# Kernel optimization log

Hardware: AMD Instinct MI355X
Metric: run time of the kernel (lower is better)

Reference implementation:

```python
import jax, jax.numpy as jnp
import numpy as np

N = 100000
C = 64
E = 3200000


def setup_inputs() -> dict:
    key = jax.random.key(0)
    k1, k2, k3 = jax.random.split(key, 3)
    edge_index = jax.random.randint(k1, (2, E), 0, N, dtype=jnp.int64)
    # nn.Linear(num_nodes, out_channels): weight [C, N], bias [C]
    W = jax.random.normal(k2, (C, N), dtype=jnp.float32) * 0.01
    b = jax.random.normal(k3, (C,), dtype=jnp.float32) * 0.01
    return {"edge_index": edge_index, "W": W, "b": b}


def reference(edge_index, W, b):
    # logits = A @ W.T + b, with A the N x N COO adjacency built from edge_index.
    # Row r of A @ W.T = sum_{edges (r, c)} W[:, c], so this is a gather of
    # W.T rows at col, segment-summed over row (duplicate edges accumulate,
    # matching torch sparse COO semantics).
    n = W.shape[1]
    row = edge_index[0]
    col = edge_index[1]
    row = row - row.min()  # faithful to the original's row normalization
    Wt = W.T  # [N, C]
    gathered = Wt[col]  # [E, C]
    out = jax.ops.segment_sum(gathered, row, num_segments=n)  # [N, C]
    return out + b
```

## Files before the change

kernel.cpp:

```cpp
#include <hip/hip_runtime.h>


#define OVF_MAX (1 << 19)
#define NBKT 512
#define BSH 9
#define SLOTS 30
#define GT_STRIDE 16
#define SL 56
#define LROWS 196

typedef unsigned int uint2_ev __attribute__((ext_vector_type(2)));
typedef unsigned int uint4_ev __attribute__((ext_vector_type(4)));

__device__ __forceinline__ float bf16u_to_f(unsigned short u) {
    union { unsigned int i; float f; } x; x.i = ((unsigned int)u) << 16; return x.f;
}
__device__ __forceinline__ float bflo(unsigned int u) {
    union { unsigned int i; float f; } x; x.i = u << 16; return x.f;
}
__device__ __forceinline__ float bfhi(unsigned int u) {
    union { unsigned int i; float f; } x; x.i = u & 0xFFFF0000u; return x.f;
}

__global__ __launch_bounds__(1024) void LINK_detect_kernel(
    const unsigned int* __restrict__ words, int E, int* __restrict__ flags,
    int* __restrict__ gtail) {
    long long twoE = 2LL * E;
    int tid = threadIdx.x;
    unsigned int oddOr = 0u;
    int nscan = (int)(twoE < 8192 ? twoE : 8192);
    for (int i = tid; i < nscan; i += blockDim.x) {
        if (i & 1) oddOr |= words[i];
        long long j = twoE - 1 - i;
        if (j >= nscan && (j & 1)) oddOr |= words[j];
    }
    __shared__ unsigned int sred[16];
    for (int off = 32; off > 0; off >>= 1)
        oddOr |= (unsigned int)__shfl_down((int)oddOr, off, 64);
    int wid = tid >> 6;
    if ((tid & 63) == 0) sred[wid] = oddOr;
    __syncthreads();
    if (tid == 0) {
        unsigned int o = 0;
        for (int i = 0; i < (int)(blockDim.x >> 6); ++i) o |= sred[i];
        flags[0] = o ? 1 : 0;
        flags[1] = 0x7f7f7f7f;
        flags[8] = 0;
    }
    for (int k = tid; k < NBKT; k += blockDim.x) gtail[k * GT_STRIDE] = 0;
}

__global__ void LINK_transpose_kernel(const float* __restrict__ W,
                                      unsigned short* __restrict__ Wtb, int N) {
    __shared__ float tile[64][65];
    int n0 = blockIdx.x * 64;
    int lx = threadIdx.x & 63;
    int ly = threadIdx.x >> 6;
#pragma unroll
    for (int it = 0; it < 16; ++it) {
        int ch = ly + 4 * it;
        float v = 0.0f;
        if (n0 + lx < N) v = W[(size_t)ch * N + (n0 + lx)];
        tile[lx][ch] = v;
    }
    __syncthreads();
#pragma unroll
    for (int it = 0; it < 16; ++it) {
        int nn = ly + 4 * it;
        if (n0 + nn <= N) {
            union { float f; unsigned int i; } x; x.f = tile[nn][lx];
            unsigned int u = x.i;
            unsigned int r = (u + 0x7fffu + ((u >> 16) & 1u)) >> 16;
            Wtb[((size_t)(n0 + nn) << 6) + lx] = (unsigned short)r;
        }
    }
}

__global__ __launch_bounds__(1024, 8) void LINK_part_kernel(
    const unsigned int* __restrict__ words, int E, int N, int segcap,
    int* __restrict__ gtail, unsigned int* __restrict__ recs,
    int* __restrict__ ovf, int* __restrict__ flags) {
    __shared__ unsigned int lstage[NBKT * SLOTS];
    __shared__ int lcnt[NBKT];
    __shared__ int sred[16];
    int tid = threadIdx.x;
    int lane = tid & 63, wid = tid >> 6;
    for (int k = tid; k < NBKT; k += 1024) lcnt[k] = 0;
    __syncthreads();
    int isInt32 = flags[0];
    int mnr = 0x7f7f7f7f;
    long long P = ((long long)E + 1) >> 1;
    long long stride = (long long)gridDim.x * 1024;
    for (long long p = (long long)blockIdx.x * 1024 + tid; p < P; p += stride) {
        long long e0 = p << 1;
        int r0, c0, r1 = 0, c1 = 0;
        bool has1 = (e0 + 1 < E);
        if (isInt32) {
            if (has1) {
                uint2_ev rr = __builtin_nontemporal_load((const uint2_ev*)(words + e0));
                uint2_ev cc = __builtin_nontemporal_load((const uint2_ev*)(words + E + e0));
                r0 = (int)rr.x; r1 = (int)rr.y; c0 = (int)cc.x; c1 = (int)cc.y;
            } else {
                r0 = (int)words[e0]; c0 = (int)words[E + e0];
            }
        } else {
            if (has1) {
                uint4_ev rr = __builtin_nontemporal_load((const uint4_ev*)(words + (e0 << 1)));
                uint4_ev cc = __builtin_nontemporal_load((const uint4_ev*)(words + 2LL * E + (e0 << 1)));
                r0 = (int)rr.x; r1 = (int)rr.z; c0 = (int)cc.x; c1 = (int)cc.z;
            } else {
                r0 = (int)words[e0 << 1]; c0 = (int)words[2LL * E + (e0 << 1)];
            }
        }
#pragma unroll
        for (int u = 0; u < 2; ++u) {
            if (u && !has1) break;
            int r = u ? r1 : r0, c = u ? c1 : c0;
            mnr = min(mnr, r);
            if ((unsigned)r < (unsigned)N && (unsigned)c < (unsigned)N) {
                int k = r & (NBKT - 1);
                unsigned int rec = ((unsigned int)(r >> BSH) << 17) | (unsigned int)c;
                int pos = atomicAdd(&lcnt[k], 1);
                if (pos < SLOTS) {
                    lstage[k * SLOTS + pos] = rec;
                } else {
                    int g = atomicAdd(&gtail[k * GT_STRIDE], 1);
                    if (g < segcap) recs[(size_t)k * segcap + g] = rec;
                    else {
                        int oi = atomicAdd(&flags[8], 1);
                        if (oi < OVF_MAX) { ovf[2 * oi] = r; ovf[2 * oi + 1] = c; }
                    }
                }
            }
        }
    }
    __syncthreads();
    for (int k = wid; k < NBKT; k += 16) {
        int cnt = lcnt[k]; if (cnt > SLOTS) cnt = SLOTS;
        if (cnt > 0) {
            int g = 0;
            if (lane == 0) g = atomicAdd(&gtail[k * GT_STRIDE], cnt);
            g = __shfl(g, 0);
            if (lane < cnt) {
                int gg = g + lane;
                unsigned int rec = lstage[k * SLOTS + lane];
                if (gg < segcap) recs[(size_t)k * segcap + gg] = rec;
                else {
                    int oi = atomicAdd(&flags[8], 1);
                    if (oi < OVF_MAX) {
                        ovf[2 * oi] = (int)((rec >> 17) << BSH) | k;
                        ovf[2 * oi + 1] = (int)(rec & 0x1FFFF);
                    }
                }
            }
        }
    }
    for (int off = 32; off > 0; off >>= 1) mnr = min(mnr, __shfl_down(mnr, off, 64));
    if (lane == 0) sred[wid] = mnr;
    __syncthreads();
    if (tid == 0) {
        int m = sred[0];
        for (int i = 1; i < 16; ++i) m = min(m, sred[i]);
        atomicMin(&flags[1], m);
    }
}

__global__ __launch_bounds__(1024, 8) void LINK_bgather_kernel(
    const int* __restrict__ gtail, const unsigned int* __restrict__ recs, int segcap,
    const unsigned short* __restrict__ Wtb, const float* __restrict__ bias,
    float* __restrict__ out, int* __restrict__ flags, int* __restrict__ ovf, int N) {
    __shared__ __attribute__((aligned(16))) int lcols[LROWS * SL];
    __shared__ int lcnt[LROWS];
    int tid = threadIdx.x;
    int lane = tid & 63, wid = tid >> 6;
    int nloc = (N + NBKT - 1) >> BSH;
    for (int b = blockIdx.x; b < NBKT; b += gridDim.x) {
        __syncthreads();
        for (int k = tid; k < nloc; k += 1024) lcnt[k] = 0;
        __syncthreads();
        int len = gtail[b * GT_STRIDE]; if (len > segcap) len = segcap;
        const unsigned int* rp = recs + (size_t)b * segcap;
        for (int i = tid; i < len; i += 1024) {
            unsigned int rec = __builtin_nontemporal_load(rp + i);
            int lr = (int)(rec >> 17);
            int c = (int)(rec & 0x1FFFF);
            int pos = atomicAdd(&lcnt[lr], 1);
            if (pos < SL) {
                lcols[lr * SL + pos] = c;
            } else {
                int oi = atomicAdd(&flags[8], 1);
                if (oi < OVF_MAX) { ovf[2 * oi] = (lr << BSH) | b; ovf[2 * oi + 1] = c; }
            }
        }
        __syncthreads();
        if (tid < nloc) {
            int c0 = lcnt[tid]; if (c0 > SL) c0 = SL;
            if (c0 & 1) { lcols[tid * SL + c0] = N; ++c0; }
            lcnt[tid] = c0;
        }
        __syncthreads();
        int rmin = flags[1];
        int half = lane >> 5, ln = lane & 31;
        const unsigned int* __restrict__ W32 = (const unsigned int*)Wtb;
        float bv = bias[(ln << 1) + half];
        for (int lr = wid; lr < nloc; lr += 16) {
            int cnt = lcnt[lr];
            int base = lr * SL;
            float aL = 0.0f, aH = 0.0f;
            int j = 0;
            for (; j + 16 <= cnt; j += 16) {
                int4 q0 = *(const int4*)&lcols[base + j + (half << 2)];
                int4 q1 = *(const int4*)&lcols[base + j + 8 + (half << 2)];
                unsigned int u0 = W32[(((unsigned)q0.x) << 5) | ln];
                unsigned int u1 = W32[(((unsigned)q0.y) << 5) | ln];
                unsigned int u2 = W32[(((unsigned)q0.z) << 5) | ln];
                unsigned int u3 = W32[(((unsigned)q0.w) << 5) | ln];
                unsigned int u4 = W32[(((unsigned)q1.x) << 5) | ln];
                unsigned int u5 = W32[(((unsigned)q1.y) << 5) | ln];
                unsigned int u6 = W32[(((unsigned)q1.z) << 5) | ln];
                unsigned int u7 = W32[(((unsigned)q1.w) << 5) | ln];
                float l0 = (bflo(u0) + bflo(u1)) + (bflo(u2) + bflo(u3));
                float l1 = (bflo(u4) + bflo(u5)) + (bflo(u6) + bflo(u7));
                float h0 = (bfhi(u0) + bfhi(u1)) + (bfhi(u2) + bfhi(u3));
                float h1 = (bfhi(u4) + bfhi(u5)) + (bfhi(u6) + bfhi(u7));
                aL += l0 + l1;
                aH += h0 + h1;
            }
            for (; j + 8 <= cnt; j += 8) {
                int4 q = *(const int4*)&lcols[base + j + (half << 2)];
                unsigned int u0 = W32[(((unsigned)q.x) << 5) | ln];
                unsigned int u1 = W32[(((unsigned)q.y) << 5) | ln];
                unsigned int u2 = W32[(((unsigned)q.z) << 5) | ln];
                unsigned int u3 = W32[(((unsigned)q.w) << 5) | ln];
                aL += (bflo(u0) + bflo(u1)) + (bflo(u2) + bflo(u3));
                aH += (bfhi(u0) + bfhi(u1)) + (bfhi(u2) + bfhi(u3));
            }
            for (; j + 4 <= cnt; j += 4) {
                int2 q = *(const int2*)&lcols[base + j + (half << 1)];
                unsigned int u0 = W32[(((unsigned)q.x) << 5) | ln];
                unsigned int u1 = W32[(((unsigned)q.y) << 5) | ln];
                aL += bflo(u0) + bflo(u1);
                aH += bfhi(u0) + bfhi(u1);
            }
            for (; j + 2 <= cnt; j += 2) {
                int c = lcols[base + j + half];
                unsigned int u = W32[(((unsigned)c) << 5) | ln];
                aL += bflo(u);
                aH += bfhi(u);
            }
            aL += __shfl_xor(aL, 32, 64);
            aH += __shfl_xor(aH, 32, 64);
            int orow = (lr << BSH) + b - rmin;
            if ((unsigned)orow < (unsigned)N)
                out[((size_t)orow << 6) + (ln << 1) + half] = (half ? aH : aL) + bv;
        }
    }
}

__global__ void LINK_tail_kernel(float* __restrict__ out, const float* __restrict__ bias,
                                 const int* __restrict__ flags, const int* __restrict__ ovf,
                                 const unsigned short* __restrict__ Wtb, int N) {
    int rmin = flags[1];
    int nloc = (N + NBKT - 1) >> BSH;
    long long start = (long long)nloc * NBKT - (long long)rmin;
    if (start < 0) start = 0;
    if (start < N) {
        long long total = ((long long)N - start) * 64;
        long long base = start * 64;
        long long i0 = (long long)blockIdx.x * blockDim.x + threadIdx.x;
        long long stride = (long long)gridDim.x * blockDim.x;
        for (long long i = i0; i < total; i += stride) out[base + i] = bias[(int)(i & 63)];
    }
    int cnt = flags[8]; if (cnt > OVF_MAX) cnt = OVF_MAX;
    if (cnt == 0) return;
    int g = blockIdx.x * blockDim.x + threadIdx.x;
    int w = g >> 6, lane = g & 63;
    int nw = (gridDim.x * blockDim.x) >> 6;
    for (int i = w; i < cnt; i += nw) {
        int r = ovf[2 * i] - rmin;
        int c = ovf[2 * i + 1];
        if ((unsigned)r >= (unsigned)N || (unsigned)c >= (unsigned)N) continue;
        atomicAdd(&out[((size_t)r << 6) + lane], bf16u_to_f(Wtb[((size_t)c << 6) + lane]));
    }
}

__global__ void LINK_initout_kernel(float* __restrict__ out, const float* __restrict__ b,
                                    int total, int* __restrict__ flags) {
    int i = blockIdx.x * blockDim.x + threadIdx.x;
    if (i == 0) { flags[0] = 0; flags[1] = 0x7fffffff; flags[2] = 0x7fffffff; }
    if (i < total) out[i] = b[i & 63];
}

__global__ __launch_bounds__(256) void LINK_analyze_kernel(
    const unsigned int* __restrict__ words, int E, int* __restrict__ flags) {
    const uint4* __restrict__ w4 = (const uint4*)words;
    int tid = blockIdx.x * blockDim.x + threadIdx.x;
    int nth = gridDim.x * blockDim.x;
    int n1 = E >> 2;
    long long twoE = 2LL * E;
    int n2 = (int)(twoE >> 2);
    unsigned int oddOr = 0u;
    int mn32 = 0x7fffffff, mn64 = 0x7fffffff;
    for (int i = tid; i < n2; i += nth) {
        uint4 w = w4[i];
        oddOr |= (w.y | w.w);
        mn64 = min(mn64, min((int)w.x, (int)w.z));
        if (i < n1)
            mn32 = min(mn32, min(min((int)w.x, (int)w.y), min((int)w.z, (int)w.w)));
    }
    for (long long i = ((long long)n1 << 2) + tid; i < E; i += nth)
        mn32 = min(mn32, (int)words[i]);
    for (long long i = ((long long)n2 << 2) + tid; i < twoE; i += nth) {
        unsigned int w = words[i];
        if (i & 1) oddOr |= w; else mn64 = min(mn64, (int)w);
    }
    for (int off = 32; off > 0; off >>= 1) {
        oddOr |= (unsigned int)__shfl_down((int)oddOr, off, 64);
        mn32 = min(mn32, __shfl_down(mn32, off, 64));
        mn64 = min(mn64, __shfl_down(mn64, off, 64));
    }
    __shared__ int s_or[4], s_m32[4], s_m64[4];
    int wid = threadIdx.x >> 6;
    if ((threadIdx.x & 63) == 0) { s_or[wid] = (int)oddOr; s_m32[wid] = mn32; s_m64[wid] = mn64; }
    __syncthreads();
    if (threadIdx.x == 0) {
        int o = s_or[0] | s_or[1] | s_or[2] | s_or[3];
        int a = min(min(s_m32[0], s_m32[1]), min(s_m32[2], s_m32[3]));
        int d = min(min(s_m64[0], s_m64[1]), min(s_m64[2], s_m64[3]));
        if (o) atomicOr(&flags[0], 1);
        atomicMin(&flags[1], a);
        atomicMin(&flags[2], d);
    }
}

__global__ void LINK_scatter_kernel(const unsigned int* __restrict__ words, int E,
                                    const float* __restrict__ W,
                                    float* __restrict__ out,
                                    const int* __restrict__ flags, int N) {
    long long g = (long long)blockIdx.x * blockDim.x + threadIdx.x;
    int e = (int)(g >> 6);
    if (e >= E) return;
    int ch = (int)(g & 63);
    int r, c, rmin;
    if (flags[0]) { r = (int)words[e]; c = (int)words[E + e]; rmin = flags[1]; }
    else { r = (int)words[2LL * e]; c = (int)words[2LL * (E + e)]; rmin = flags[2]; }
    r -= rmin;
    if ((unsigned)r >= (unsigned)N || (unsigned)c >= (unsigned)N) return;
    atomicAdd(&out[((size_t)r << 6) + ch], W[(size_t)ch * N + c]);
}

static inline size_t align256(size_t x) { return (x + 255) & ~(size_t)255; }

extern "C" void kernel_launch(void* const* d_in, const int* in_sizes, int n_in,
                              void* d_out, int out_size, void* d_ws, size_t ws_size,
                              hipStream_t stream) {
    const unsigned int* words = (const unsigned int*)d_in[0];
    const float* W = (const float*)d_in[1];
    const float* b = (const float*)d_in[2];
    float* out = (float*)d_out;

    int E = in_sizes[0] / 2;
    int N = in_sizes[1] / 64;
    int total = out_size;

    size_t off_flags = 0;
    size_t off_wtb   = align256(off_flags + 256 * sizeof(int));
    size_t off_gtail = align256(off_wtb + (size_t)(N + 1) * 64 * sizeof(unsigned short));
    size_t off_ovf   = align256(off_gtail + (size_t)NBKT * GT_STRIDE * sizeof(int));
    size_t off_recs  = align256(off_ovf + (size_t)OVF_MAX * 2 * sizeof(int));

    int* flags = (int*)((char*)d_ws + off_flags);
    unsigned short* Wtb = (unsigned short*)((char*)d_ws + off_wtb);
    int* gtail = (int*)((char*)d_ws + off_gtail);
    int* ovf   = (int*)((char*)d_ws + off_ovf);
    unsigned int* recs = (unsigned int*)((char*)d_ws + off_recs);

    long long avail = (ws_size > off_recs)
        ? (long long)((ws_size - off_recs) / ((size_t)NBKT * sizeof(int))) : 0;
    int segcap = (int)(avail > 16384 ? 16384 : avail);
    int avg = E / NBKT + 1;
    int nloc = (N + NBKT - 1) >> BSH;
    bool useMain = (nloc <= LROWS) && (E > 0) &&
                   (segcap >= avg + avg / 8 + 64);

    if (useMain) {
        LINK_detect_kernel<<<1, 1024, 0, stream>>>(words, E, flags, gtail);
        LINK_transpose_kernel<<<(N + 64) / 64, 256, 0, stream>>>(W, Wtb, N);
        LINK_part_kernel<<<NBKT, 1024, 0, stream>>>(words, E, N, segcap,
                                                    gtail, recs, ovf, flags);
        LINK_bgather_kernel<<<NBKT, 1024, 0, stream>>>(gtail, recs, segcap, Wtb, b,
                                                       out, flags, ovf, N);
        LINK_tail_kernel<<<64, 256, 0, stream>>>(out, b, flags, ovf, Wtb, N);
    } else {
        LINK_initout_kernel<<<(total + 255) / 256, 256, 0, stream>>>(out, b, total, flags);
        LINK_analyze_kernel<<<256, 256, 0, stream>>>(words, E, flags);
        long long tthreads = (long long)E * 64;
        LINK_scatter_kernel<<<(int)((tthreads + 255) / 256), 256, 0, stream>>>(
            words, E, W, out, flags, N);
    }
}
```

Measured before the change: 196.7 us.

## Fuse detect into transpose kernel and fold tail work into gather's last block

Merges the single-block detect/init kernel into the transpose launch as an extra block 0, cutting one kernel launch. It removes the separate tail kernel by writing bias to wrapped rows inside the gather and having the last-finishing block, found with an atomic counter and threadfence, apply overflow atomics. The gather now handles exactly one bucket per block. The trade-off is that overflow handling runs on a single block, which would be slow if overflow is large. Ordering is correct only because block 0 initializes flags before the later kernels read them.

```diff
diff --git a/kernel.cpp b/kernel.cpp
--- a/kernel.cpp
+++ b/kernel.cpp
@@ -22,40 +22,40 @@
     union { unsigned int i; float f; } x; x.i = u & 0xFFFF0000u; return x.f;
 }
 
-__global__ __launch_bounds__(1024) void LINK_detect_kernel(
+__global__ __launch_bounds__(256) void LINK_prep_kernel(
     const unsigned int* __restrict__ words, int E, int* __restrict__ flags,
-    int* __restrict__ gtail) {
-    long long twoE = 2LL * E;
+    int* __restrict__ gtail, const float* __restrict__ W,
+    unsigned short* __restrict__ Wtb, int N) {
     int tid = threadIdx.x;
-    unsigned int oddOr = 0u;
-    int nscan = (int)(twoE < 8192 ? twoE : 8192);
-    for (int i = tid; i < nscan; i += blockDim.x) {
-        if (i & 1) oddOr |= words[i];
-        long long j = twoE - 1 - i;
-        if (j >= nscan && (j & 1)) oddOr |= words[j];
-    }
-    __shared__ unsigned int sred[16];
-    for (int off = 32; off > 0; off >>= 1)
-        oddOr |= (unsigned int)__shfl_down((int)oddOr, off, 64);
-    int wid = tid >> 6;
-    if ((tid & 63) == 0) sred[wid] = oddOr;
-    __syncthreads();
-    if (tid == 0) {
-        unsigned int o = 0;
-        for (int i = 0; i < (int)(blockDim.x >> 6); ++i) o |= sred[i];
-        flags[0] = o ? 1 : 0;
-        flags[1] = 0x7f7f7f7f;
-        flags[8] = 0;
-    }
-    for (int k = tid; k < NBKT; k += blockDim.x) gtail[k * GT_STRIDE] = 0;
-}
-
-__global__ void LINK_transpose_kernel(const float* __restrict__ W,
-                                      unsigned short* __restrict__ Wtb, int N) {
+    if (blockIdx.x == 0) {
+        long long twoE = 2LL * E;
+        unsigned int oddOr = 0u;
+        int nscan = (int)(twoE < 8192 ? twoE : 8192);
+        for (int i = tid; i < nscan; i += 256) {
+            if (i & 1) oddOr |= words[i];
+            long long j = twoE - 1 - i;
+            if (j >= nscan && (j & 1)) oddOr |= words[j];
+        }
+        __shared__ unsigned int sred[4];
+        for (int off = 32; off > 0; off >>= 1)
+            oddOr |= (unsigned int)__shfl_down((int)oddOr, off, 64);
+        int wid = tid >> 6;
+        if ((tid & 63) == 0) sred[wid] = oddOr;
+        __syncthreads();
+        if (tid == 0) {
+            unsigned int o = sred[0] | sred[1] | sred[2] | sred[3];
+            flags[0] = o ? 1 : 0;
+            flags[1] = 0x7f7f7f7f;
+            flags[8] = 0;
+            flags[9] = 0;
+        }
+        for (int k = tid; k < NBKT; k += 256) gtail[k * GT_STRIDE] = 0;
+        return;
+    }
     __shared__ float tile[64][65];
-    int n0 = blockIdx.x * 64;
-    int lx = threadIdx.x & 63;
-    int ly = threadIdx.x >> 6;
+    int n0 = (blockIdx.x - 1) * 64;
+    int lx = tid & 63;
+    int ly = tid >> 6;
 #pragma unroll
     for (int it = 0; it < 16; ++it) {
         int ch = ly + 4 * it;
@@ -171,12 +171,13 @@
     float* __restrict__ out, int* __restrict__ flags, int* __restrict__ ovf, int N) {
     __shared__ __attribute__((aligned(16))) int lcols[LROWS * SL];
     __shared__ int lcnt[LROWS];
+    __shared__ int isLast;
     int tid = threadIdx.x;
     int lane = tid & 63, wid = tid >> 6;
     int nloc = (N + NBKT - 1) >> BSH;
-    for (int b = blockIdx.x; b < NBKT; b += gridDim.x) {
-        __syncthreads();
-        for (int k = tid; k < nloc; k += 1024) lcnt[k] = 0;
+    int b = blockIdx.x;
+    {
+        if (tid < nloc) lcnt[tid] = 0;
         __syncthreads();
         int len = gtail[b * GT_STRIDE]; if (len > segcap) len = segcap;
         const unsigned int* rp = recs + (size_t)b * segcap;
@@ -250,37 +251,33 @@
             }
             aL += __shfl_xor(aL, 32, 64);
             aH += __shfl_xor(aH, 32, 64);
-            int orow = (lr << BSH) + b - rmin;
-            if ((unsigned)orow < (unsigned)N)
-                out[((size_t)orow << 6) + (ln << 1) + half] = (half ? aH : aL) + bv;
-        }
-    }
-}
-
-__global__ void LINK_tail_kernel(float* __restrict__ out, const float* __restrict__ bias,
-                                 const int* __restrict__ flags, const int* __restrict__ ovf,
-                                 const unsigned short* __restrict__ Wtb, int N) {
-    int rmin = flags[1];
-    int nloc = (N + NBKT - 1) >> BSH;
-    long long start = (long long)nloc * NBKT - (long long)rmin;
-    if (start < 0) start = 0;
-    if (start < N) {
-        long long total = ((long long)N - start) * 64;
-        long long base = start * 64;
-        long long i0 = (long long)blockIdx.x * blockDim.x + threadIdx.x;
-        long long stride = (long long)gridDim.x * blockDim.x;
-        for (long long i = i0; i < total; i += stride) out[base + i] = bias[(int)(i & 63)];
-    }
-    int cnt = flags[8]; if (cnt > OVF_MAX) cnt = OVF_MAX;
-    if (cnt == 0) return;
-    int g = blockIdx.x * blockDim.x + threadIdx.x;
-    int w = g >> 6, lane = g & 63;
-    int nw = (gridDim.x * blockDim.x) >> 6;
-    for (int i = w; i < cnt; i += nw) {
-        int r = ovf[2 * i] - rmin;
-        int c = ovf[2 * i + 1];
-        if ((unsigned)r >= (unsigned)N || (unsigned)c >= (unsigned)N) continue;
-        atomicAdd(&out[((size_t)r << 6) + lane], bf16u_to_f(Wtb[((size_t)c << 6) + lane]));
+            int r = (lr << BSH) + b;
+            int orow = r - rmin;
+            if (orow >= 0) {
+                if (orow < N)
+                    out[((size_t)orow << 6) + (ln << 1) + half] = (half ? aH : aL) + bv;
+            } else {
+                int o2 = r + (nloc << BSH) - rmin;
+                if (o2 < N)
+                    out[((size_t)o2 << 6) + (ln << 1) + half] = bv;
+            }
+        }
+    }
+    __threadfence();
+    if (tid == 0) isLast = (atomicAdd(&flags[9], 1) == (int)gridDim.x - 1);
+    __syncthreads();
+    if (isLast) {
+        __threadfence();
+        int cnt = flags[8]; if (cnt > OVF_MAX) cnt = OVF_MAX;
+        if (cnt > 0) {
+            int rmin = flags[1];
+            for (int i = wid; i < cnt; i += 16) {
+                int r = ovf[2 * i] - rmin;
+                int c = ovf[2 * i + 1];
+                if ((unsigned)r >= (unsigned)N || (unsigned)c >= (unsigned)N) continue;
+                atomicAdd(&out[((size_t)r << 6) + lane], bf16u_to_f(Wtb[((size_t)c << 6) + lane]));
+            }
+        }
     }
 }
 
@@ -384,13 +381,12 @@
                    (segcap >= avg + avg / 8 + 64);
 
     if (useMain) {
-        LINK_detect_kernel<<<1, 1024, 0, stream>>>(words, E, flags, gtail);
-        LINK_transpose_kernel<<<(N + 64) / 64, 256, 0, stream>>>(W, Wtb, N);
+        int T = (N + 64) / 64;
+        LINK_prep_kernel<<<T + 1, 256, 0, stream>>>(words, E, flags, gtail, W, Wtb, N);
         LINK_part_kernel<<<NBKT, 1024, 0, stream>>>(words, E, N, segcap,
                                                     gtail, recs, ovf, flags);
         LINK_bgather_kernel<<<NBKT, 1024, 0, stream>>>(gtail, recs, segcap, Wtb, b,
                                                        out, flags, ovf, N);
-        LINK_tail_kernel<<<64, 256, 0, stream>>>(out, b, flags, ovf, Wtb, N);
     } else {
         LINK_initout_kernel<<<(total + 255) / 256, 256, 0, stream>>>(out, b, total, flags);
         LINK_analyze_kernel<<<256, 256, 0, stream>>>(words, E, flags);
```

After: 435.1 us. 2.21x slower.
